# Optimization experiments

Measured on AMD Instinct MI355X. Metric: run time of the kernel, lower is better.

The kernel has to match this reference:

```python
import jax, jax.numpy as jnp
import numpy as np

N = 50000          # nodes
E = 400000         # edges
F = 128            # num_features
CUTOFF = 5.0       # cutoff_dist
NUM_RBF = 20
EPS = 1e-8


def setup_inputs() -> dict:
    key = jax.random.key(0)
    ks = jax.random.split(key, 10)
    v = jax.random.normal(ks[0], (N, F, 3), dtype=jnp.float32)
    s = jax.random.normal(ks[1], (N, F), dtype=jnp.float32)
    js = jax.random.randint(ks[2], (E,), 0, N)
    r_vec = jax.random.normal(ks[3], (E, 3), dtype=jnp.float32) * 2.0
    # r layout: [col0 unused, col1 = js index (stored as float), cols 2:5 = 3-vector]
    r = jnp.concatenate([jnp.zeros((E, 1), jnp.float32),
                         js.astype(jnp.float32)[:, None],
                         r_vec], axis=1)
    W1 = jax.random.normal(ks[4], (F, F), dtype=jnp.float32) * 0.05
    b1 = jnp.zeros((F,), jnp.float32)
    W2 = jax.random.normal(ks[5], (F, 3 * F), dtype=jnp.float32) * 0.05
    b2 = jnp.zeros((3 * F,), jnp.float32)
    Wr = jax.random.normal(ks[6], (NUM_RBF, 3 * F), dtype=jnp.float32) * 0.05
    br = jnp.zeros((3 * F,), jnp.float32)
    return {"v": v, "s": s, "r": r, "W1": W1, "b1": b1,
            "W2": W2, "b2": b2, "Wr": Wr, "br": br}


def reference(v, s, r, W1, b1, W2, b2, Wr, br):
    js = r[:, 1].astype(jnp.int32)              # [E]
    r_vectors = r[:, 2:]                        # [E,3]

    # s_path: Linear -> SiLU -> Linear
    phi = jax.nn.silu(s @ W1 + b1) @ W2 + b2    # [N,3F]

    # RBF — faithful to source bug: slices [:,2:] of the already-sliced
    # r_vectors, so only |z| enters the RBF.
    norm_z = jnp.abs(r_vectors[:, 2:3])         # [E,1]
    n = jnp.arange(1, NUM_RBF + 1, dtype=jnp.float32)[None, :]  # [1,20]
    rbf = jnp.sin(n * (jnp.pi / CUTOFF) * norm_z) / (norm_z + EPS)  # [E,20]

    # r_path linear then cosine cutoff applied elementwise to its output
    x = rbf @ Wr + br                           # [E,3F]
    W = 0.5 * (jnp.cos(jnp.pi * x / CUTOFF) + 1.0) * (x < CUTOFF).astype(x.dtype)

    pre = phi[js] * W                           # gather + gate, [E,3F]
    s1 = pre[:, :F]
    s2 = pre[:, F:2 * F]
    s3 = pre[:, 2 * F:]

    dirn = r_vectors / (jnp.linalg.norm(r_vectors, axis=1, keepdims=True) + EPS)  # [E,3]
    left_2 = v[js] * s1[:, :, None] + s3[:, :, None] * dirn[:, None, :]  # [E,F,3]

    delta_v = jnp.zeros_like(v).at[js].add(left_2)   # scatter-add [N,F,3]
    delta_s = jnp.zeros_like(s).at[js].add(s2)       # scatter-add [N,F]
    return delta_v, delta_s
```

## Files before the change

kernel.cpp:

```cpp
#include <hip/hip_runtime.h>
#include <math.h>

#define NN 50000
#define NE 400000
#define FF 128
#define PD 384
#define NRBF 20
#define CUT 5.0f
#define EPSV 1e-8f
#define PI_F 3.14159265358979323846f
#define FEATW 24
#define HLP 144

typedef __attribute__((ext_vector_type(8))) short bf16x8;
typedef __attribute__((ext_vector_type(4))) float f32x4;

static __device__ __forceinline__ short f2bf(float x)
{
    union { float f; unsigned u; } c; c.f = x;
    unsigned r = c.u + 0x7FFFu + ((c.u >> 16) & 1u);
    return (short)(r >> 16);
}

__global__ void prep_wt(const float* __restrict__ W1, const float* __restrict__ W2,
                        short* __restrict__ WT1, short* __restrict__ WT2)
{
    int idx = blockIdx.x * 256 + threadIdx.x;
    if (idx < FF * FF) {
        int c = idx >> 7, k = idx & 127;
        WT1[c * FF + k] = f2bf(W1[k * FF + c]);
    } else if (idx < FF * FF + PD * FF) {
        int i2 = idx - FF * FF;
        int c = i2 >> 7, k = i2 & 127;
        WT2[c * FF + k] = f2bf(W2[(size_t)k * PD + c]);
    }
}

__global__ __launch_bounds__(256) void phi_mfma(
    const float* __restrict__ s, const short* __restrict__ WT1,
    const float* __restrict__ b1, const short* __restrict__ WT2,
    const float* __restrict__ b2, float* __restrict__ phi)
{
    __shared__ short Hl[64][HLP];

    const int tid  = threadIdx.x;
    const int wv   = tid >> 6;
    const int lane = tid & 63;
    const int lr   = lane & 15;
    const int lk   = lane >> 4;
    const int node0 = blockIdx.x * 64;
    const int rowA  = node0 + wv * 16 + lr;
    const bool rowAok = rowA < NN;

    bf16x8 a[4];
#pragma unroll
    for (int kk = 0; kk < 4; kk++) {
        const float* sp = s + (size_t)rowA * FF + kk * 32 + lk * 8;
        float4 u0 = make_float4(0.f, 0.f, 0.f, 0.f);
        float4 u1 = make_float4(0.f, 0.f, 0.f, 0.f);
        if (rowAok) { u0 = *(const float4*)sp; u1 = *(const float4*)(sp + 4); }
        bf16x8 t;
        t[0] = f2bf(u0.x); t[1] = f2bf(u0.y); t[2] = f2bf(u0.z); t[3] = f2bf(u0.w);
        t[4] = f2bf(u1.x); t[5] = f2bf(u1.y); t[6] = f2bf(u1.z); t[7] = f2bf(u1.w);
        a[kk] = t;
    }

    f32x4 acc1[8];
#pragma unroll
    for (int ct = 0; ct < 8; ct++) acc1[ct] = (f32x4){0.f, 0.f, 0.f, 0.f};

#pragma unroll
    for (int ct = 0; ct < 8; ct++) {
        const short* wp = WT1 + (ct * 16 + lr) * FF + lk * 8;
#pragma unroll
        for (int kk = 0; kk < 4; kk++) {
            bf16x8 b = *(const bf16x8*)(wp + kk * 32);
            acc1[ct] = __builtin_amdgcn_mfma_f32_16x16x32_bf16(a[kk], b, acc1[ct], 0, 0, 0);
        }
    }

#pragma unroll
    for (int ct = 0; ct < 8; ct++) {
        const int col = ct * 16 + lr;
        const float bias = b1[col];
#pragma unroll
        for (int q = 0; q < 4; q++) {
            float x = acc1[ct][q] + bias;
            float h = x / (1.f + __expf(-x));
            Hl[wv * 16 + lk * 4 + q][col] = f2bf(h);
        }
    }
    __syncthreads();

    bf16x8 a2[4];
#pragma unroll
    for (int kk = 0; kk < 4; kk++)
        a2[kk] = *(const bf16x8*)&Hl[wv * 16 + lr][kk * 32 + lk * 8];

    const int rowD0 = node0 + wv * 16 + lk * 4;
    for (int ct = 0; ct < 24; ct++) {
        f32x4 acc = {0.f, 0.f, 0.f, 0.f};
        const short* wp = WT2 + (ct * 16 + lr) * FF + lk * 8;
#pragma unroll
        for (int kk = 0; kk < 4; kk++) {
            bf16x8 b = *(const bf16x8*)(wp + kk * 32);
            acc = __builtin_amdgcn_mfma_f32_16x16x32_bf16(a2[kk], b, acc, 0, 0, 0);
        }
        const int col = ct * 16 + lr;
        const float bias = b2[col];
#pragma unroll
        for (int q = 0; q < 4; q++) {
            int row = rowD0 + q;
            if (row < NN) phi[(size_t)row * PD + col] = acc[q] + bias;
        }
    }
}

__global__ void count_kernel(const float* __restrict__ r, int* __restrict__ counts)
{
    int e = blockIdx.x * 256 + threadIdx.x;
    if (e < NE) {
        int j = (int)r[(size_t)e * 5 + 1];
        atomicAdd(&counts[j], 1);
    }
}

__global__ __launch_bounds__(1024) void scan_kernel(
    const int* __restrict__ counts, int* __restrict__ offsets, int* __restrict__ cursor)
{
    const int PER = (NN + 1023) / 1024;
    const int tid = threadIdx.x;
    const int start = tid * PER;

    int local = 0;
    for (int k = 0; k < PER; k++) {
        int i = start + k;
        if (i < NN) local += counts[i];
    }
    int lane = tid & 63, wv = tid >> 6;
    int vsc = local;
#pragma unroll
    for (int off = 1; off < 64; off <<= 1) {
        int t = __shfl_up(vsc, off);
        if (lane >= off) vsc += t;
    }
    __shared__ int wsum[16], wpre[16];
    if (lane == 63) wsum[wv] = vsc;
    __syncthreads();
    if (tid == 0) {
        int run = 0;
        for (int w = 0; w < 16; w++) { wpre[w] = run; run += wsum[w]; }
    }
    __syncthreads();
    int run = (vsc - local) + wpre[wv];
    for (int k = 0; k < PER; k++) {
        int i = start + k;
        if (i < NN) {
            offsets[i] = run;
            cursor[i]  = run;
            run += counts[i];
        }
    }
    if (tid == 1023) offsets[NN] = run;
}

__global__ void fill_edge_kernel(const float* __restrict__ r,
                                 int* __restrict__ cursor,
                                 float* __restrict__ feat)
{
    int e = blockIdx.x * 256 + threadIdx.x;
    if (e >= NE) return;
    const float* re = r + (size_t)e * 5;
    int j = (int)re[1];
    float rx = re[2], ry = re[3], rz = re[4];
    int p = atomicAdd(&cursor[j], 1);

    float nz = fabsf(rz);
    float inv = 1.f / (sqrtf(rx * rx + ry * ry + rz * rz) + EPSV);
    float rcp = 1.f / (nz + EPSV);
    float arg = (PI_F / CUT) * nz;

    float fbuf[FEATW];
#pragma unroll
    for (int n = 0; n < NRBF; n++)
        fbuf[n] = sinf((float)(n + 1) * arg) * rcp;
    fbuf[20] = rx * inv;
    fbuf[21] = ry * inv;
    fbuf[22] = rz * inv;
    fbuf[23] = 0.f;

    float* dst = feat + (size_t)p * FEATW;
#pragma unroll
    for (int q = 0; q < 6; q++)
        *(float4*)(dst + q * 4) = *(const float4*)(fbuf + q * 4);
}

__global__ __launch_bounds__(128) void node_kernel(
    const float* __restrict__ v, const float* __restrict__ phi,
    const float* __restrict__ Wr, const float* __restrict__ br,
    const int* __restrict__ offsets, const float* __restrict__ feat,
    float* __restrict__ out_v, float* __restrict__ out_s)
{
    const int i = blockIdx.x;
    const int f = threadIdx.x;
    const int e0 = offsets[i], e1 = offsets[i + 1];

    float wra[NRBF], wrb[NRBF], wrc[NRBF];
#pragma unroll
    for (int n = 0; n < NRBF; n++) {
        wra[n] = Wr[n * PD + f];
        wrb[n] = Wr[n * PD + FF + f];
        wrc[n] = Wr[n * PD + 2 * FF + f];
    }
    const float xba = br[f], xbb = br[FF + f], xbc = br[2 * FF + f];

    float aW0 = 0.f, aW1 = 0.f, aD0 = 0.f, aD1 = 0.f, aD2 = 0.f;

    __shared__ __align__(16) float lds_feat[16][FEATW];

    for (int base = e0; base < e1; base += 16) {
        int nb = min(16, e1 - base);
        __syncthreads();
        if (f < nb * 6) {
            int slot = f / 6, q = f % 6;
            *(float4*)&lds_feat[slot][q * 4] =
                *(const float4*)(feat + (size_t)(base + slot) * FEATW + q * 4);
        }
        __syncthreads();

#pragma unroll 2
        for (int jj = 0; jj < nb; jj++) {
            float rb[NRBF];
#pragma unroll
            for (int q = 0; q < 5; q++) {
                float4 t = *(const float4*)&lds_feat[jj][q * 4];
                rb[q * 4]     = t.x; rb[q * 4 + 1] = t.y;
                rb[q * 4 + 2] = t.z; rb[q * 4 + 3] = t.w;
            }
            float4 dv = *(const float4*)&lds_feat[jj][20];

            float xa = xba, xb = xbb, xc = xbc;
#pragma unroll
            for (int n = 0; n < NRBF; n++) {
                xa = fmaf(rb[n], wra[n], xa);
                xb = fmaf(rb[n], wrb[n], xb);
                xc = fmaf(rb[n], wrc[n], xc);
            }
            float Wa = (xa < CUT) ? 0.5f * (__cosf((PI_F / CUT) * xa) + 1.f) : 0.f;
            float Wb = (xb < CUT) ? 0.5f * (__cosf((PI_F / CUT) * xb) + 1.f) : 0.f;
            float Wc = (xc < CUT) ? 0.5f * (__cosf((PI_F / CUT) * xc) + 1.f) : 0.f;
            aW0 += Wa;
            aW1 += Wb;
            aD0 = fmaf(Wc, dv.x, aD0);
            aD1 = fmaf(Wc, dv.y, aD1);
            aD2 = fmaf(Wc, dv.z, aD2);
        }
    }

    const float pa = phi[(size_t)i * PD + f];
    const float pb = phi[(size_t)i * PD + FF + f];
    const float pc = phi[(size_t)i * PD + 2 * FF + f];
    const float s1s = pa * aW0;

    const float v0 = v[(size_t)i * PD + f * 3 + 0];
    const float v1 = v[(size_t)i * PD + f * 3 + 1];
    const float v2 = v[(size_t)i * PD + f * 3 + 2];

    __shared__ float ov[PD];
    ov[f * 3 + 0] = fmaf(v0, s1s, pc * aD0);
    ov[f * 3 + 1] = fmaf(v1, s1s, pc * aD1);
    ov[f * 3 + 2] = fmaf(v2, s1s, pc * aD2);
    __syncthreads();
    out_v[(size_t)i * PD + f]          = ov[f];
    out_v[(size_t)i * PD + FF + f]     = ov[FF + f];
    out_v[(size_t)i * PD + 2 * FF + f] = ov[2 * FF + f];
    out_s[(size_t)i * FF + f] = pb * aW1;
}

extern "C" void kernel_launch(void* const* d_in, const int* in_sizes, int n_in,
                              void* d_out, int out_size, void* d_ws, size_t ws_size,
                              hipStream_t stream)
{
    const float* v  = (const float*)d_in[0];
    const float* s  = (const float*)d_in[1];
    const float* r  = (const float*)d_in[2];
    const float* W1 = (const float*)d_in[3];
    const float* b1 = (const float*)d_in[4];
    const float* W2 = (const float*)d_in[5];
    const float* b2 = (const float*)d_in[6];
    const float* Wr = (const float*)d_in[7];
    const float* br = (const float*)d_in[8];

    float* out_v = (float*)d_out;
    float* out_s = out_v + (size_t)NN * PD;

    char* ws = (char*)d_ws;
    size_t off = 0;
    float* phi    = (float*)(ws + off); off += (size_t)NN * PD * 4;
    float* feat   = (float*)(ws + off); off += (size_t)NE * FEATW * 4;
    int*   counts = (int*)(ws + off);   off += (size_t)NN * 4;
    int*   cursor = (int*)(ws + off);   off += (size_t)NN * 4;
    int*   offsets= (int*)(ws + off);   off += (size_t)(NN + 1) * 4;
    short* WT1    = (short*)(ws + off); off += (size_t)FF * FF * 2;
    short* WT2    = (short*)(ws + off); off += (size_t)PD * FF * 2;

    hipMemsetAsync(counts, 0, (size_t)NN * 4, stream);
    prep_wt<<<(FF * FF + PD * FF + 255) / 256, 256, 0, stream>>>(W1, W2, WT1, WT2);
    phi_mfma<<<(NN + 63) / 64, 256, 0, stream>>>(s, WT1, b1, WT2, b2, phi);
    count_kernel<<<(NE + 255) / 256, 256, 0, stream>>>(r, counts);
    scan_kernel<<<1, 1024, 0, stream>>>(counts, offsets, cursor);
    fill_edge_kernel<<<(NE + 255) / 256, 256, 0, stream>>>(r, cursor, feat);
    node_kernel<<<NN, 128, 0, stream>>>(v, phi, Wr, br, offsets, feat,
                                        out_v, out_s);
}
```

Measured before the change: 533.5 us.

## Batch nodes per block, parallelize offset scan, prepack MFMA weight fragments

The node kernel now handles 16 nodes per block. It stages up to 192 edges of features into LDS at once and falls back to global reads past that, which reduces per-node Wr register loads and block launch overhead. The single-block 1024-thread scan becomes a three-kernel multi-block scan. MFMA B operands are pre-swizzled so each lane makes one contiguous 16-byte load. The trade-offs are less block-level parallelism and uncoalesced strided out_v stores in place of the LDS transpose.

```diff
diff --git a/kernel.cpp b/kernel.cpp
--- a/kernel.cpp
+++ b/kernel.cpp
@@ -11,6 +11,10 @@
 #define PI_F 3.14159265358979323846f
 #define FEATW 24
 #define HLP 144
+#define SCH 1024
+#define NB ((NN + SCH - 1) / SCH)
+#define GN 16
+#define WEDGE 192
 
 typedef __attribute__((ext_vector_type(8))) short bf16x8;
 typedef __attribute__((ext_vector_type(4))) float f32x4;
@@ -23,22 +27,34 @@
 }
 
 __global__ void prep_wt(const float* __restrict__ W1, const float* __restrict__ W2,
-                        short* __restrict__ WT1, short* __restrict__ WT2)
+                        short* __restrict__ WT1p, short* __restrict__ WT2p)
 {
     int idx = blockIdx.x * 256 + threadIdx.x;
-    if (idx < FF * FF) {
-        int c = idx >> 7, k = idx & 127;
-        WT1[c * FF + k] = f2bf(W1[k * FF + c]);
-    } else if (idx < FF * FF + PD * FF) {
-        int i2 = idx - FF * FF;
-        int c = i2 >> 7, k = i2 & 127;
-        WT2[c * FF + k] = f2bf(W2[(size_t)k * PD + c]);
+    if (idx < 32 * 64) {
+        int frag = idx >> 6, lane = idx & 63;
+        int ct = frag >> 2, kk = frag & 3;
+        int c  = ct * 16 + (lane & 15);
+        int k0 = kk * 32 + (lane >> 4) * 8;
+        short* dst = WT1p + (size_t)idx * 8;
+#pragma unroll
+        for (int j = 0; j < 8; j++)
+            dst[j] = f2bf(W1[(size_t)(k0 + j) * FF + c]);
+    } else if (idx < 32 * 64 + 96 * 64) {
+        int id2 = idx - 32 * 64;
+        int frag = id2 >> 6, lane = id2 & 63;
+        int ct = frag >> 2, kk = frag & 3;
+        int c  = ct * 16 + (lane & 15);
+        int k0 = kk * 32 + (lane >> 4) * 8;
+        short* dst = WT2p + (size_t)id2 * 8;
+#pragma unroll
+        for (int j = 0; j < 8; j++)
+            dst[j] = f2bf(W2[(size_t)(k0 + j) * PD + c]);
     }
 }
 
 __global__ __launch_bounds__(256) void phi_mfma(
-    const float* __restrict__ s, const short* __restrict__ WT1,
-    const float* __restrict__ b1, const short* __restrict__ WT2,
+    const float* __restrict__ s, const short* __restrict__ WT1p,
+    const float* __restrict__ b1, const short* __restrict__ WT2p,
     const float* __restrict__ b2, float* __restrict__ phi)
 {
     __shared__ short Hl[64][HLP];
@@ -68,13 +84,11 @@
     f32x4 acc1[8];
 #pragma unroll
     for (int ct = 0; ct < 8; ct++) acc1[ct] = (f32x4){0.f, 0.f, 0.f, 0.f};
-
 #pragma unroll
     for (int ct = 0; ct < 8; ct++) {
-        const short* wp = WT1 + (ct * 16 + lr) * FF + lk * 8;
 #pragma unroll
         for (int kk = 0; kk < 4; kk++) {
-            bf16x8 b = *(const bf16x8*)(wp + kk * 32);
+            bf16x8 b = *(const bf16x8*)(WT1p + ((size_t)(ct * 4 + kk) * 64 + lane) * 8);
             acc1[ct] = __builtin_amdgcn_mfma_f32_16x16x32_bf16(a[kk], b, acc1[ct], 0, 0, 0);
         }
     }
@@ -100,10 +114,9 @@
     const int rowD0 = node0 + wv * 16 + lk * 4;
     for (int ct = 0; ct < 24; ct++) {
         f32x4 acc = {0.f, 0.f, 0.f, 0.f};
-        const short* wp = WT2 + (ct * 16 + lr) * FF + lk * 8;
 #pragma unroll
         for (int kk = 0; kk < 4; kk++) {
-            bf16x8 b = *(const bf16x8*)(wp + kk * 32);
+            bf16x8 b = *(const bf16x8*)(WT2p + ((size_t)(ct * 4 + kk) * 64 + lane) * 8);
             acc = __builtin_amdgcn_mfma_f32_16x16x32_bf16(a2[kk], b, acc, 0, 0, 0);
         }
         const int col = ct * 16 + lr;
@@ -125,43 +138,79 @@
     }
 }
 
-__global__ __launch_bounds__(1024) void scan_kernel(
-    const int* __restrict__ counts, int* __restrict__ offsets, int* __restrict__ cursor)
-{
-    const int PER = (NN + 1023) / 1024;
-    const int tid = threadIdx.x;
-    const int start = tid * PER;
-
-    int local = 0;
-    for (int k = 0; k < PER; k++) {
-        int i = start + k;
-        if (i < NN) local += counts[i];
-    }
-    int lane = tid & 63, wv = tid >> 6;
-    int vsc = local;
-#pragma unroll
-    for (int off = 1; off < 64; off <<= 1) {
-        int t = __shfl_up(vsc, off);
-        if (lane >= off) vsc += t;
-    }
-    __shared__ int wsum[16], wpre[16];
-    if (lane == 63) wsum[wv] = vsc;
-    __syncthreads();
-    if (tid == 0) {
-        int run = 0;
-        for (int w = 0; w < 16; w++) { wpre[w] = run; run += wsum[w]; }
-    }
-    __syncthreads();
-    int run = (vsc - local) + wpre[wv];
-    for (int k = 0; k < PER; k++) {
-        int i = start + k;
-        if (i < NN) {
-            offsets[i] = run;
-            cursor[i]  = run;
-            run += counts[i];
-        }
-    }
-    if (tid == 1023) offsets[NN] = run;
+__global__ __launch_bounds__(256) void scan1(
+    const int* __restrict__ counts, int* __restrict__ offsets, int* __restrict__ bsum)
+{
+    const int t = threadIdx.x;
+    const int base = blockIdx.x * SCH + t * 4;
+    int4 c = make_int4(0, 0, 0, 0);
+    if (base + 3 < NN) c = *(const int4*)(counts + base);
+    else {
+        if (base     < NN) c.x = counts[base];
+        if (base + 1 < NN) c.y = counts[base + 1];
+        if (base + 2 < NN) c.z = counts[base + 2];
+    }
+    int s0 = c.x, s1 = s0 + c.y, s2 = s1 + c.z, s3 = s2 + c.w;
+    int lane = t & 63, wv = t >> 6;
+    int inc = s3;
+#pragma unroll
+    for (int o = 1; o < 64; o <<= 1) {
+        int u = __shfl_up(inc, o);
+        if (lane >= o) inc += u;
+    }
+    __shared__ int ws[4];
+    if (lane == 63) ws[wv] = inc;
+    __syncthreads();
+    int wp = 0;
+    for (int w = 0; w < wv; w++) wp += ws[w];
+    int ex = wp + inc - s3;
+    int4 o4 = make_int4(ex, ex + s0, ex + s1, ex + s2);
+    if (base + 3 < NN) *(int4*)(offsets + base) = o4;
+    else {
+        if (base     < NN) offsets[base]     = o4.x;
+        if (base + 1 < NN) offsets[base + 1] = o4.y;
+        if (base + 2 < NN) offsets[base + 2] = o4.z;
+    }
+    __syncthreads();
+    if (t == 0) bsum[blockIdx.x] = ws[0] + ws[1] + ws[2] + ws[3];
+}
+
+__global__ void scan2(const int* __restrict__ bsum, int* __restrict__ bpre,
+                      int* __restrict__ offsets)
+{
+    int t = threadIdx.x;
+    int vl = (t < NB) ? bsum[t] : 0;
+    int inc = vl;
+#pragma unroll
+    for (int o = 1; o < 64; o <<= 1) {
+        int u = __shfl_up(inc, o);
+        if (t >= o) inc += u;
+    }
+    if (t < NB) bpre[t] = inc - vl;
+    if (t == 63) offsets[NN] = inc;
+}
+
+__global__ __launch_bounds__(256) void scan3(
+    int* __restrict__ offsets, int* __restrict__ cursor, const int* __restrict__ bpre)
+{
+    const int t = threadIdx.x;
+    const int base = blockIdx.x * SCH + t * 4;
+    const int add = bpre[blockIdx.x];
+    if (base + 3 < NN) {
+        int4 o = *(const int4*)(offsets + base);
+        o.x += add; o.y += add; o.z += add; o.w += add;
+        *(int4*)(offsets + base) = o;
+        *(int4*)(cursor  + base) = o;
+    } else {
+#pragma unroll
+        for (int k = 0; k < 4; k++) {
+            if (base + k < NN) {
+                int x = offsets[base + k] + add;
+                offsets[base + k] = x;
+                cursor[base + k]  = x;
+            }
+        }
+    }
 }
 
 __global__ void fill_edge_kernel(const float* __restrict__ r,
@@ -201,9 +250,22 @@
     const int* __restrict__ offsets, const float* __restrict__ feat,
     float* __restrict__ out_v, float* __restrict__ out_s)
 {
-    const int i = blockIdx.x;
-    const int f = threadIdx.x;
-    const int e0 = offsets[i], e1 = offsets[i + 1];
+    const int f  = threadIdx.x;
+    const int i0 = blockIdx.x * GN;
+
+    __shared__ int offs[GN + 1];
+    __shared__ __align__(16) float lf[WEDGE][FEATW];
+
+    if (f <= GN) offs[f] = offsets[i0 + f];
+    __syncthreads();
+
+    const int eBase = offs[0];
+    const int nSt = min(offs[GN] - eBase, WEDGE);
+    for (int idx = f; idx < nSt * 6; idx += 128) {
+        int sl = idx / 6, q = idx % 6;
+        *(float4*)&lf[sl][q * 4] =
+            *(const float4*)(feat + (size_t)(eBase + sl) * FEATW + q * 4);
+    }
 
     float wra[NRBF], wrb[NRBF], wrc[NRBF];
 #pragma unroll
@@ -213,31 +275,34 @@
         wrc[n] = Wr[n * PD + 2 * FF + f];
     }
     const float xba = br[f], xbb = br[FF + f], xbc = br[2 * FF + f];
-
-    float aW0 = 0.f, aW1 = 0.f, aD0 = 0.f, aD1 = 0.f, aD2 = 0.f;
-
-    __shared__ __align__(16) float lds_feat[16][FEATW];
-
-    for (int base = e0; base < e1; base += 16) {
-        int nb = min(16, e1 - base);
-        __syncthreads();
-        if (f < nb * 6) {
-            int slot = f / 6, q = f % 6;
-            *(float4*)&lds_feat[slot][q * 4] =
-                *(const float4*)(feat + (size_t)(base + slot) * FEATW + q * 4);
-        }
-        __syncthreads();
-
-#pragma unroll 2
-        for (int jj = 0; jj < nb; jj++) {
+    __syncthreads();
+
+    for (int nd = 0; nd < GN; nd++) {
+        const int e0 = offs[nd], e1 = offs[nd + 1];
+        float aW0 = 0.f, aW1 = 0.f, aD0 = 0.f, aD1 = 0.f, aD2 = 0.f;
+
+        for (int ep = e0; ep < e1; ++ep) {
+            int rel = ep - eBase;
             float rb[NRBF];
-#pragma unroll
-            for (int q = 0; q < 5; q++) {
-                float4 t = *(const float4*)&lds_feat[jj][q * 4];
-                rb[q * 4]     = t.x; rb[q * 4 + 1] = t.y;
-                rb[q * 4 + 2] = t.z; rb[q * 4 + 3] = t.w;
+            float4 dv;
+            if (rel < WEDGE) {
+#pragma unroll
+                for (int q = 0; q < 5; q++) {
+                    float4 t = *(const float4*)&lf[rel][q * 4];
+                    rb[q * 4]     = t.x; rb[q * 4 + 1] = t.y;
+                    rb[q * 4 + 2] = t.z; rb[q * 4 + 3] = t.w;
+                }
+                dv = *(const float4*)&lf[rel][20];
+            } else {
+                const float* fp = feat + (size_t)ep * FEATW;
+#pragma unroll
+                for (int q = 0; q < 5; q++) {
+                    float4 t = *(const float4*)(fp + q * 4);
+                    rb[q * 4]     = t.x; rb[q * 4 + 1] = t.y;
+                    rb[q * 4 + 2] = t.z; rb[q * 4 + 3] = t.w;
+                }
+                dv = *(const float4*)(fp + 20);
             }
-            float4 dv = *(const float4*)&lds_feat[jj][20];
 
             float xa = xba, xb = xbb, xc = xbc;
 #pragma unroll
@@ -255,26 +320,19 @@
             aD1 = fmaf(Wc, dv.y, aD1);
             aD2 = fmaf(Wc, dv.z, aD2);
         }
-    }
-
-    const float pa = phi[(size_t)i * PD + f];
-    const float pb = phi[(size_t)i * PD + FF + f];
-    const float pc = phi[(size_t)i * PD + 2 * FF + f];
-    const float s1s = pa * aW0;
-
-    const float v0 = v[(size_t)i * PD + f * 3 + 0];
-    const float v1 = v[(size_t)i * PD + f * 3 + 1];
-    const float v2 = v[(size_t)i * PD + f * 3 + 2];
-
-    __shared__ float ov[PD];
-    ov[f * 3 + 0] = fmaf(v0, s1s, pc * aD0);
-    ov[f * 3 + 1] = fmaf(v1, s1s, pc * aD1);
-    ov[f * 3 + 2] = fmaf(v2, s1s, pc * aD2);
-    __syncthreads();
-    out_v[(size_t)i * PD + f]          = ov[f];
-    out_v[(size_t)i * PD + FF + f]     = ov[FF + f];
-    out_v[(size_t)i * PD + 2 * FF + f] = ov[2 * FF + f];
-    out_s[(size_t)i * FF + f] = pb * aW1;
+
+        const int i = i0 + nd;
+        const float pa = phi[(size_t)i * PD + f];
+        const float pb = phi[(size_t)i * PD + FF + f];
+        const float pc = phi[(size_t)i * PD + 2 * FF + f];
+        const float s1s = pa * aW0;
+        const float* vp = v + (size_t)i * PD + f * 3;
+        float* op = out_v + (size_t)i * PD + f * 3;
+        op[0] = fmaf(vp[0], s1s, pc * aD0);
+        op[1] = fmaf(vp[1], s1s, pc * aD1);
+        op[2] = fmaf(vp[2], s1s, pc * aD2);
+        out_s[(size_t)i * FF + f] = pb * aW1;
+    }
 }
 
 extern "C" void kernel_launch(void* const* d_in, const int* in_sizes, int n_in,
@@ -301,15 +359,19 @@
     int*   counts = (int*)(ws + off);   off += (size_t)NN * 4;
     int*   cursor = (int*)(ws + off);   off += (size_t)NN * 4;
     int*   offsets= (int*)(ws + off);   off += (size_t)(NN + 1) * 4;
-    short* WT1    = (short*)(ws + off); off += (size_t)FF * FF * 2;
-    short* WT2    = (short*)(ws + off); off += (size_t)PD * FF * 2;
+    int*   bsum   = (int*)(ws + off);   off += (size_t)64 * 4;
+    int*   bpre   = (int*)(ws + off);   off += (size_t)64 * 4;
+    short* WT1p   = (short*)(ws + off); off += (size_t)32 * 64 * 8 * 2;
+    short* WT2p   = (short*)(ws + off); off += (size_t)96 * 64 * 8 * 2;
 
     hipMemsetAsync(counts, 0, (size_t)NN * 4, stream);
-    prep_wt<<<(FF * FF + PD * FF + 255) / 256, 256, 0, stream>>>(W1, W2, WT1, WT2);
-    phi_mfma<<<(NN + 63) / 64, 256, 0, stream>>>(s, WT1, b1, WT2, b2, phi);
+    prep_wt<<<32, 256, 0, stream>>>(W1, W2, WT1p, WT2p);
+    phi_mfma<<<(NN + 63) / 64, 256, 0, stream>>>(s, WT1p, b1, WT2p, b2, phi);
     count_kernel<<<(NE + 255) / 256, 256, 0, stream>>>(r, counts);
-    scan_kernel<<<1, 1024, 0, stream>>>(counts, offsets, cursor);
+    scan1<<<NB, 256, 0, stream>>>(counts, offsets, bsum);
+    scan2<<<1, 64, 0, stream>>>(bsum, bpre, offsets);
+    scan3<<<NB, 256, 0, stream>>>(offsets, cursor, bpre);
     fill_edge_kernel<<<(NE + 255) / 256, 256, 0, stream>>>(r, cursor, feat);
-    node_kernel<<<NN, 128, 0, stream>>>(v, phi, Wr, br, offsets, feat,
-                                        out_v, out_s);
-}
+    node_kernel<<<NN / GN, 128, 0, stream>>>(v, phi, Wr, br, offsets, feat,
+                                             out_v, out_s);
+}
```

New measurement: 431.7 us. -19.1%, faster.
